# Kernel tuning notes

Hardware: AMD Instinct MI355X
Metric: run time of the kernel (lower is better)

The kernel has to match this reference:

```python
import jax, jax.numpy as jnp
import numpy as np
from jax import lax

RESI_RATIO = 0.5  # abs(quant_resi=-0.5)
BETA = 0.25


def setup_inputs() -> dict:
    key = jax.random.key(0)
    k1, k2, k3, k4 = jax.random.split(key, 4)
    B, C, T, H, W = 2, 32, 8, 32, 32
    V = 8192
    f_BCTHW = jax.random.normal(k1, (B, C, T, H, W), dtype=jnp.float32)
    emb_weight = jax.random.normal(k2, (V, C), dtype=jnp.float32)
    conv_w = jax.random.normal(k3, (C, C, 3, 3, 3), dtype=jnp.float32) * 0.02
    conv_b = jax.random.normal(k4, (C,), dtype=jnp.float32) * 0.02
    return {"f_BCTHW": f_BCTHW, "emb_weight": emb_weight, "conv_w": conv_w, "conv_b": conv_b}


def _mse(a, b):
    d = a - b
    return jnp.mean(d * d)


def reference(f_BCTHW, emb_weight, conv_w, conv_b):
    f = f_BCTHW.astype(jnp.float32)
    B, C, T, H, W = f.shape
    V = emb_weight.shape[0]

    # ---- nearest-codebook assignment (vocab_norm=False path) ----
    # query uses detached f (stop_gradient) exactly as torch .detach()
    q = lax.stop_gradient(f).transpose(0, 2, 3, 4, 1).reshape(-1, C)  # [N, C]
    emb_sg = lax.stop_gradient(emb_weight)
    # ||q||^2 + ||e||^2 - 2 q.e  (addmm_ with alpha=-2, beta=1)
    dist = (jnp.sum(q * q, axis=1, keepdims=True)
            + jnp.sum(emb_sg * emb_sg, axis=1)
            - 2.0 * (q @ emb_sg.T))  # [N, V]
    idx_N = jnp.argmin(dist, axis=1)  # [N] int

    # ---- usage stats (bincount) ----
    counts = jnp.zeros((V,), jnp.float32).at[idx_N].add(1.0)
    prob = counts / jnp.sum(counts)
    vocab_usage = jnp.mean((prob > (0.01 / V)).astype(jnp.float32)) * 100.0

    # ---- embedding gather + residual conv blend ----
    fh = emb_weight[idx_N].reshape(B, T, H, W, C).transpose(0, 4, 1, 2, 3)  # [B,C,T,H,W]
    conv = lax.conv_general_dilated(
        fh, conv_w, window_strides=(1, 1, 1), padding='SAME',
        dimension_numbers=('NCDHW', 'OIDHW', 'NCDHW'))
    conv = conv + conv_b[None, :, None, None, None]
    fh = fh * (1.0 - RESI_RATIO) + conv * RESI_RATIO

    # ---- VQ loss + straight-through estimator ----
    vq_loss = BETA * _mse(lax.stop_gradient(fh), f) + _mse(fh, lax.stop_gradient(f))
    fhat = lax.stop_gradient(fh - f) + f

    return fhat, vq_loss, vocab_usage
```

## Files before the change

kernel.cpp:

```cpp
#include <hip/hip_runtime.h>

#define NQ    16384
#define CDIM  32
#define VSZ   8192
#define PLANE 8192
#define BSTR  262144
#define NEL   524288
#define MARGIN 0.010f
#define NSEG  32
#define GUARD 1088

typedef unsigned long long u64;
typedef unsigned int u32;
typedef unsigned short u16;
using f32x4 = __attribute__((ext_vector_type(4))) float;
using s16x8 = __attribute__((ext_vector_type(8))) short;

__device__ __forceinline__ u32 flip_bits(u32 b) {
    return (b & 0x80000000u) ? ~b : (b | 0x80000000u);
}
__device__ __forceinline__ float unflip_val(u32 b) {
    u32 u = (b & 0x80000000u) ? (b ^ 0x80000000u) : ~b;
    return __uint_as_float(u);
}
__device__ __forceinline__ u16 bf16_rne(float x) {
    u32 u = __float_as_uint(x);
    return (u16)((u + 0x7fffu + ((u >> 16) & 1u)) >> 16);
}

__global__ void k_prep(const float* __restrict__ f, const float* __restrict__ emb,
                       const float* __restrict__ cw,
                       u16* __restrict__ EFh, u16* __restrict__ EFl,
                       u16* __restrict__ QFh, u16* __restrict__ QFl,
                       u16* __restrict__ WFh, u16* __restrict__ WFl,
                       float* __restrict__ enorm, int* __restrict__ counts,
                       int* __restrict__ uct) {
    int t = blockIdx.x * 256 + threadIdx.x;
    if (t < 32768) {
        int tile = t >> 6, l = t & 63;
        int row = tile * 16 + (l & 15);
        int k0 = (l >> 4) * 8;
        const float* src = emb + row * CDIM + k0;
        s16x8 vh, vl;
#pragma unroll
        for (int i = 0; i < 8; ++i) {
            float v = src[i];
            u16 hb = bf16_rne(v);
            float hf = __uint_as_float(((u32)hb) << 16);
            vh[i] = (short)hb;
            vl[i] = (short)bf16_rne(v - hf);
        }
        *(s16x8*)(EFh + t * 8) = vh;
        *(s16x8*)(EFl + t * 8) = vl;
    } else if (t < 98304) {
        int t2 = t - 32768;
        int st = t2 >> 6, l = t2 & 63;
        int n = st * 16 + (l & 15);
        int k0 = (l >> 4) * 8;
        int b = n >> 13, p = n & (PLANE - 1);
        const float* fq = f + b * BSTR + p;
        s16x8 vh, vl;
#pragma unroll
        for (int i = 0; i < 8; ++i) {
            float v = -2.0f * fq[(k0 + i) * PLANE];
            u16 hb = bf16_rne(v);
            float hf = __uint_as_float(((u32)hb) << 16);
            vh[i] = (short)hb;
            vl[i] = (short)bf16_rne(v - hf);
        }
        *(s16x8*)(QFh + t2 * 8) = vh;
        *(s16x8*)(QFl + t2 * 8) = vl;
    } else if (t < 106496) {
        int j = t - 98304;
        const float4* row = (const float4*)(emb + j * CDIM);
        float s = 0.f;
#pragma unroll
        for (int r = 0; r < 8; ++r) {
            float4 v = row[r];
            s += v.x * v.x + v.y * v.y + v.z * v.z + v.w * v.w;
        }
        enorm[j] = s;
        counts[j] = 0;
        if (j == 0) { *uct = 0; }
    } else if (t < 109952) {
        int i = t - 106496;
        int nt = i >> 6, l = i & 63;
        int col = nt * 16 + (l & 15);
        int co = col & 31, u = col >> 5;
        int k0 = (l >> 4) * 8;
        s16x8 vh, vl;
#pragma unroll
        for (int j = 0; j < 8; ++j) {
            int ci = k0 + j;
            float v = cw[co * 864 + ci * 27 + u];
            u16 hb = bf16_rne(v);
            float hf = __uint_as_float(((u32)hb) << 16);
            vh[j] = (short)hb;
            vl[j] = (short)bf16_rne(v - hf);
        }
        *(s16x8*)(WFh + i * 8) = vh;
        *(s16x8*)(WFl + i * 8) = vl;
    }
}

__global__ __launch_bounds__(64) void k_mfma3(
    const u16* __restrict__ QFh, const u16* __restrict__ QFl,
    const u16* __restrict__ EFh, const u16* __restrict__ EFl,
    const float* __restrict__ enorm,
    u64* __restrict__ PARTK, float* __restrict__ PARTM2) {
    const int l = threadIdx.x;
    const int lq = (l >> 4) * 4;
    const int wq = blockIdx.x >> 5, seg = blockIdx.x & 31;

    s16x8 qh[4], ql[4];
#pragma unroll
    for (int s = 0; s < 4; ++s) {
        int st = wq * 4 + s;
        qh[s] = *(const s16x8*)(QFh + (st * 64 + l) * 8);
        ql[s] = *(const s16x8*)(QFl + (st * 64 + l) * 8);
    }
    float m1v[4] = {1e30f, 1e30f, 1e30f, 1e30f};
    float m2v[4] = {1e30f, 1e30f, 1e30f, 1e30f};
    int   m1i[4] = {0, 0, 0, 0};

#pragma unroll 2
    for (int t = 0; t < 16; ++t) {
        int tile = seg * 16 + t;
        s16x8 ah = *(const s16x8*)(EFh + (tile * 64 + l) * 8);
        s16x8 al = *(const s16x8*)(EFl + (tile * 64 + l) * 8);
        f32x4 en = *(const f32x4*)(enorm + tile * 16 + lq);
        int bc = tile * 16 + lq;
#pragma unroll
        for (int s = 0; s < 4; ++s) {
            f32x4 acc = __builtin_amdgcn_mfma_f32_16x16x32_bf16(ah, qh[s], en, 0, 0, 0);
            acc = __builtin_amdgcn_mfma_f32_16x16x32_bf16(ah, ql[s], acc, 0, 0, 0);
            acc = __builtin_amdgcn_mfma_f32_16x16x32_bf16(al, qh[s], acc, 0, 0, 0);
#pragma unroll
            for (int r = 0; r < 4; ++r) {
                float v = acc[r];
                bool lt = v < m1v[s];
                float m2c = fminf(m2v[s], v);
                m2v[s] = lt ? m1v[s] : m2c;
                m1i[s] = lt ? (bc + r) : m1i[s];
                m1v[s] = fminf(m1v[s], v);
            }
        }
    }
#pragma unroll
    for (int s = 0; s < 4; ++s) {
        u64 key = ((u64)flip_bits(__float_as_uint(m1v[s])) << 32) | (u32)m1i[s];
        float m2 = m2v[s];
#pragma unroll
        for (int off = 16; off <= 32; off <<= 1) {
            u64 ko = __shfl_xor(key, off, 64);
            float m2o = __shfl_xor(m2, off, 64);
            u64 kmax = ko > key ? ko : key;
            m2 = fminf(fminf(m2, m2o), unflip_val((u32)(kmax >> 32)));
            key = ko < key ? ko : key;
        }
        if (l < 16) {
            int q = wq * 64 + s * 16 + l;
            PARTK[seg * NQ + q] = key;
            PARTM2[seg * NQ + q] = m2;
        }
    }
}

__global__ void k_final(const u64* __restrict__ PARTK, const float* __restrict__ PARTM2,
                        int* __restrict__ out_idx, int* __restrict__ counts,
                        int* __restrict__ uct, int* __restrict__ ulist) {
    int q = blockIdx.x * 256 + threadIdx.x;
    u64 K = PARTK[q]; float M2 = PARTM2[q];
#pragma unroll
    for (int s = 1; s < NSEG; ++s) {
        u64 k = PARTK[s * NQ + q]; float m2 = PARTM2[s * NQ + q];
        u64 kmax = k > K ? k : K;
        M2 = fminf(fminf(M2, m2), unflip_val((u32)(kmax >> 32)));
        K = k < K ? k : K;
    }
    int idx = (int)(K & 0xffffffffull);
    out_idx[q] = idx;
    float m1 = unflip_val((u32)(K >> 32));
    if (M2 - m1 > MARGIN) {
        atomicAdd(&counts[idx], 1);
    } else {
        int p = atomicAdd(uct, 1);
        ulist[p] = q;
    }
}

__global__ __launch_bounds__(256) void k_exact(
    const int* __restrict__ ulist, const int* __restrict__ uct,
    const float* __restrict__ f, const float* __restrict__ emb,
    const float* __restrict__ enorm, int* __restrict__ out_idx,
    int* __restrict__ counts) {
    __shared__ u64 wred[4][2];
    const int tid = threadIdx.x;
    const int uc = *uct;
    for (int base = blockIdx.x * 2; base < uc; base += 256) {
        int nq = uc - base; if (nq > 2) nq = 2;
        int q0 = ulist[base];
        int q1 = (nq > 1) ? ulist[base + 1] : q0;
        float qv0[CDIM], qv1[CDIM];
        {
            const float* f0 = f + (q0 >> 13) * BSTR + (q0 & (PLANE - 1));
            const float* f1 = f + (q1 >> 13) * BSTR + (q1 & (PLANE - 1));
#pragma unroll
            for (int c = 0; c < CDIM; ++c) {
                qv0[c] = -2.0f * f0[c * PLANE];
                qv1[c] = -2.0f * f1[c * PLANE];
            }
        }
        u64 k0 = ~0ull, k1 = ~0ull;
        for (int jj = 0; jj < 32; ++jj) {
            int j = tid + 256 * jj;
            const float4* er = (const float4*)(emb + j * CDIM);
            float d0 = enorm[j], d1 = d0;
#pragma unroll
            for (int c4 = 0; c4 < 8; ++c4) {
                float4 v = er[c4];
                d0 = fmaf(qv0[c4 * 4 + 0], v.x, d0); d0 = fmaf(qv0[c4 * 4 + 1], v.y, d0);
                d0 = fmaf(qv0[c4 * 4 + 2], v.z, d0); d0 = fmaf(qv0[c4 * 4 + 3], v.w, d0);
                d1 = fmaf(qv1[c4 * 4 + 0], v.x, d1); d1 = fmaf(qv1[c4 * 4 + 1], v.y, d1);
                d1 = fmaf(qv1[c4 * 4 + 2], v.z, d1); d1 = fmaf(qv1[c4 * 4 + 3], v.w, d1);
            }
            u64 nk0 = ((u64)flip_bits(__float_as_uint(d0)) << 32) | (u32)j;
            u64 nk1 = ((u64)flip_bits(__float_as_uint(d1)) << 32) | (u32)j;
            if (nk0 < k0) k0 = nk0;
            if (nk1 < k1) k1 = nk1;
        }
#pragma unroll
        for (int off = 1; off <= 32; off <<= 1) {
            u64 o0 = __shfl_xor(k0, off, 64); if (o0 < k0) k0 = o0;
            u64 o1 = __shfl_xor(k1, off, 64); if (o1 < k1) k1 = o1;
        }
        if ((tid & 63) == 0) { wred[tid >> 6][0] = k0; wred[tid >> 6][1] = k1; }
        __syncthreads();
        if (tid == 0) {
            u64 b0 = wred[0][0], b1 = wred[0][1];
#pragma unroll
            for (int w = 1; w < 4; ++w) {
                if (wred[w][0] < b0) b0 = wred[w][0];
                if (wred[w][1] < b1) b1 = wred[w][1];
            }
            int i0 = (int)(b0 & 0xffffffffull);
            out_idx[q0] = i0; atomicAdd(&counts[i0], 1);
            if (nq > 1) {
                int i1 = (int)(b1 & 0xffffffffull);
                out_idx[q1] = i1; atomicAdd(&counts[i1], 1);
            }
        }
        __syncthreads();
    }
}

__global__ void k_fh2(const int* __restrict__ idx, const float* __restrict__ emb,
                      u16* __restrict__ FH2h, u16* __restrict__ FH2l,
                      const int* __restrict__ counts, float* __restrict__ out) {
    __shared__ int us[4];
    int t = blockIdx.x * 256 + threadIdx.x;
    if (t < NQ) {
        int id = idx[t];
        const float4* e = (const float4*)(emb + id * CDIM);
        s16x8 vh[4], vl[4];
#pragma unroll
        for (int r = 0; r < 8; ++r) {
            float4 v = e[r];
            float vv[4] = {v.x, v.y, v.z, v.w};
#pragma unroll
            for (int j = 0; j < 4; ++j) {
                int q = r * 4 + j;
                u16 hb = bf16_rne(vv[j]);
                float hf = __uint_as_float(((u32)hb) << 16);
                vh[q >> 3][q & 7] = (short)hb;
                vl[q >> 3][q & 7] = (short)bf16_rne(vv[j] - hf);
            }
        }
        u16* dh_ = FH2h + t * CDIM;
        u16* dl_ = FH2l + t * CDIM;
#pragma unroll
        for (int r = 0; r < 4; ++r) {
            *(s16x8*)(dh_ + r * 8) = vh[r];
            *(s16x8*)(dl_ + r * 8) = vl[r];
        }
    } else if (t < 20736) {
        int g = t - NQ;
        int r = g / 1088, off = (g % 1088) * 16;
        u32* dst;
        if (r == 0)      dst = (u32*)(FH2h - GUARD * CDIM);
        else if (r == 1) dst = (u32*)(FH2h + NQ * CDIM);
        else if (r == 2) dst = (u32*)(FH2l - GUARD * CDIM);
        else             dst = (u32*)(FH2l + NQ * CDIM);
#pragma unroll
        for (int i = 0; i < 16; ++i) dst[off + i] = 0;
    } else {
        int tid = threadIdx.x;
        int used = 0;
#pragma unroll
        for (int r = 0; r < 32; ++r) used += (counts[tid + 256 * r] > 0) ? 1 : 0;
#pragma unroll
        for (int off = 32; off > 0; off >>= 1) used += __shfl_down(used, off, 64);
        if ((tid & 63) == 0) us[tid >> 6] = used;
        __syncthreads();
        if (tid == 0) {
            int u = us[0] + us[1] + us[2] + us[3];
            out[NEL + 1] = ((float)u / (float)VSZ) * 100.0f;
        }
    }
}

__global__ __launch_bounds__(192) void k_convm2(
    const u16* __restrict__ FH2h, const u16* __restrict__ FH2l,
    const u16* __restrict__ WFh, const u16* __restrict__ WFl,
    const int* __restrict__ idx, const float* __restrict__ emb,
    const float* __restrict__ bias, const float* __restrict__ f,
    float* __restrict__ out) {
    __shared__ float part[3][64][4];
    const int l = threadIdx.x & 63;
    const int wv = threadIdx.x >> 6;
    const int ntile = blockIdx.x >> 1, cot = blockIdx.x & 1;
    const int co = cot * 16 + (l & 15);
    const int k0 = (l >> 4) * 8;

    const int nA = ntile * 16 + (l & 15);
    const int pA = nA & (PLANE - 1);
    const int tA = pA >> 10, hA = (pA >> 5) & 31, wA = pA & 31;
    const u16* pAh = FH2h + nA * CDIM + k0;
    const u16* pAl = FH2l + nA * CDIM + k0;

    const int ddt = wv - 1;
    const bool okt = ((unsigned)(tA + ddt) < 8u);

    f32x4 a0 = {0.f, 0.f, 0.f, 0.f}, a1 = a0, a2 = a0;
    const s16x8 zf = {0, 0, 0, 0, 0, 0, 0, 0};
#pragma unroll
    for (int v = 0; v < 9; ++v) {
        const int dh = v / 3 - 1, dw = v % 3 - 1;
        const int u = wv * 9 + v;
        const int du = ddt * 1024 + dh * 32 + dw;
        bool ok = okt && ((unsigned)(hA + dh) < 32u) && ((unsigned)(wA + dw) < 32u);
        s16x8 ah = *(const s16x8*)(pAh + du * CDIM);
        s16x8 al = *(const s16x8*)(pAl + du * CDIM);
        if (!ok) { ah = zf; al = zf; }
        int nt = 2 * u + cot;
        s16x8 bh = *(const s16x8*)(WFh + (nt * 64 + l) * 8);
        s16x8 bl = *(const s16x8*)(WFl + (nt * 64 + l) * 8);
        a0 = __builtin_amdgcn_mfma_f32_16x16x32_bf16(ah, bh, a0, 0, 0, 0);
        a1 = __builtin_amdgcn_mfma_f32_16x16x32_bf16(ah, bl, a1, 0, 0, 0);
        a2 = __builtin_amdgcn_mfma_f32_16x16x32_bf16(al, bh, a2, 0, 0, 0);
    }
#pragma unroll
    for (int r = 0; r < 4; ++r) part[wv][l][r] = a0[r] + a1[r] + a2[r];
    __syncthreads();
    if (wv != 0) return;

    f32x4 acc;
#pragma unroll
    for (int r = 0; r < 4; ++r)
        acc[r] = part[0][l][r] + part[1][l][r] + part[2][l][r];
    const float bv = bias[co];

    const int n0 = ntile * 16 + (l >> 4) * 4;
    const int b = n0 >> 13, p0 = n0 & (PLANE - 1);
    const long fb = (long)b * BSTR + (long)co * PLANE + p0;
    const float4 f4 = *(const float4*)(f + fb);
    const int4 iv = *(const int4*)(idx + n0);
    float o0 = 0.5f * emb[iv.x * CDIM + co] + 0.5f * (acc[0] + bv);
    float o1 = 0.5f * emb[iv.y * CDIM + co] + 0.5f * (acc[1] + bv);
    float o2 = 0.5f * emb[iv.z * CDIM + co] + 0.5f * (acc[2] + bv);
    float o3 = 0.5f * emb[iv.w * CDIM + co] + 0.5f * (acc[3] + bv);
    float4 o4 = {o0, o1, o2, o3};
    *(float4*)(out + fb) = o4;
    float d0 = o0 - f4.x, d1 = o1 - f4.y, d2 = o2 - f4.z, d3 = o3 - f4.w;
    float s = fmaf(d0, d0, fmaf(d1, d1, fmaf(d2, d2, d3 * d3)));
#pragma unroll
    for (int off = 32; off > 0; off >>= 1) s += __shfl_down(s, off, 64);
    if (l == 0) atomicAdd(out + NEL, s * (1.25f / (float)NEL));
}

extern "C" void kernel_launch(void* const* d_in, const int* in_sizes, int n_in,
                              void* d_out, int out_size, void* d_ws, size_t ws_size,
                              hipStream_t stream) {
    const float* f      = (const float*)d_in[0];
    const float* emb    = (const float*)d_in[1];
    const float* conv_w = (const float*)d_in[2];
    const float* conv_b = (const float*)d_in[3];
    float* out = (float*)d_out;
    float* ws = (float*)d_ws;

    float* enorm    = ws;
    int*   counts   = (int*)(ws + 8192);
    int*   idxb     = (int*)(ws + 16384);
    int*   uct      = (int*)(ws + 32769);
    int*   ulist    = (int*)(ws + 32772);
    u16*   EFh      = (u16*)(ws + 49408);
    u16*   EFl      = (u16*)(ws + 180480);
    u16*   QFh      = (u16*)(ws + 311552);
    u16*   QFl      = (u16*)(ws + 573696);
    u16*   WFh      = (u16*)(ws + 835840);
    u16*   WFl      = (u16*)(ws + 842752);
    u64*   PARTK    = (u64*)(ws + 849664);
    float* PARTM2   = ws + 1898240;
    u16*   FH2h     = (u16*)(ws + 849664)  + GUARD * CDIM;
    u16*   FH2l     = (u16*)(ws + 1146624) + GUARD * CDIM;

    k_prep   <<<430, 256, 0, stream>>>(f, emb, conv_w, EFh, EFl, QFh, QFl,
                                       WFh, WFl, enorm, counts, uct);
    k_mfma3  <<<8192, 64, 0, stream>>>(QFh, QFl, EFh, EFl, enorm, PARTK, PARTM2);
    k_final  <<<64, 256, 0, stream>>>(PARTK, PARTM2, idxb, counts, uct, ulist);
    k_exact  <<<128, 256, 0, stream>>>(ulist, uct, f, emb, enorm, idxb, counts);
    k_fh2    <<<82, 256, 0, stream>>>(idxb, emb, FH2h, FH2l, counts, out);
    k_convm2 <<<2048, 192, 0, stream>>>(FH2h, FH2l, WFh, WFl, idxb, emb,
                                        conv_b, f, out);
}
```

Before: 183.2 us.

## Fuse exact-recheck pass into final reduction kernel with per-block shared uncertain list

```diff
diff --git a/kernel.cpp b/kernel.cpp
--- a/kernel.cpp
+++ b/kernel.cpp
@@ -33,8 +33,7 @@
                        u16* __restrict__ EFh, u16* __restrict__ EFl,
                        u16* __restrict__ QFh, u16* __restrict__ QFl,
                        u16* __restrict__ WFh, u16* __restrict__ WFl,
-                       float* __restrict__ enorm, int* __restrict__ counts,
-                       int* __restrict__ uct) {
+                       float* __restrict__ enorm, int* __restrict__ counts) {
     int t = blockIdx.x * 256 + threadIdx.x;
     if (t < 32768) {
         int tile = t >> 6, l = t & 63;
@@ -81,7 +80,6 @@
         }
         enorm[j] = s;
         counts[j] = 0;
-        if (j == 0) { *uct = 0; }
     } else if (t < 109952) {
         int i = t - 106496;
         int nt = i >> 6, l = i & 63;
@@ -166,10 +164,19 @@
     }
 }
 
-__global__ void k_final(const u64* __restrict__ PARTK, const float* __restrict__ PARTM2,
-                        int* __restrict__ out_idx, int* __restrict__ counts,
-                        int* __restrict__ uct, int* __restrict__ ulist) {
-    int q = blockIdx.x * 256 + threadIdx.x;
+__global__ __launch_bounds__(256) void k_finalx(
+    const u64* __restrict__ PARTK, const float* __restrict__ PARTM2,
+    const float* __restrict__ f, const float* __restrict__ emb,
+    const float* __restrict__ enorm,
+    int* __restrict__ out_idx, int* __restrict__ counts) {
+    __shared__ int ulist_s[256];
+    __shared__ int ucnt_s;
+    __shared__ u64 wred[4];
+    const int tid = threadIdx.x;
+    if (tid == 0) ucnt_s = 0;
+    __syncthreads();
+
+    int q = blockIdx.x * 256 + tid;
     u64 K = PARTK[q]; float M2 = PARTM2[q];
 #pragma unroll
     for (int s = 1; s < NSEG; ++s) {
@@ -184,71 +191,45 @@
     if (M2 - m1 > MARGIN) {
         atomicAdd(&counts[idx], 1);
     } else {
-        int p = atomicAdd(uct, 1);
-        ulist[p] = q;
-    }
-}
-
-__global__ __launch_bounds__(256) void k_exact(
-    const int* __restrict__ ulist, const int* __restrict__ uct,
-    const float* __restrict__ f, const float* __restrict__ emb,
-    const float* __restrict__ enorm, int* __restrict__ out_idx,
-    int* __restrict__ counts) {
-    __shared__ u64 wred[4][2];
-    const int tid = threadIdx.x;
-    const int uc = *uct;
-    for (int base = blockIdx.x * 2; base < uc; base += 256) {
-        int nq = uc - base; if (nq > 2) nq = 2;
-        int q0 = ulist[base];
-        int q1 = (nq > 1) ? ulist[base + 1] : q0;
-        float qv0[CDIM], qv1[CDIM];
-        {
-            const float* f0 = f + (q0 >> 13) * BSTR + (q0 & (PLANE - 1));
-            const float* f1 = f + (q1 >> 13) * BSTR + (q1 & (PLANE - 1));
-#pragma unroll
-            for (int c = 0; c < CDIM; ++c) {
-                qv0[c] = -2.0f * f0[c * PLANE];
-                qv1[c] = -2.0f * f1[c * PLANE];
-            }
-        }
-        u64 k0 = ~0ull, k1 = ~0ull;
+        int p = atomicAdd(&ucnt_s, 1);
+        ulist_s[p] = q;
+    }
+    __syncthreads();
+
+    const int uc = ucnt_s;
+    for (int i = 0; i < uc; ++i) {
+        int qu = ulist_s[i];
+        const float* fq = f + (qu >> 13) * BSTR + (qu & (PLANE - 1));
+        float qv[CDIM];
+#pragma unroll
+        for (int c = 0; c < CDIM; ++c) qv[c] = -2.0f * fq[c * PLANE];
+        u64 k0 = ~0ull;
         for (int jj = 0; jj < 32; ++jj) {
             int j = tid + 256 * jj;
             const float4* er = (const float4*)(emb + j * CDIM);
-            float d0 = enorm[j], d1 = d0;
+            float d0 = enorm[j];
 #pragma unroll
             for (int c4 = 0; c4 < 8; ++c4) {
                 float4 v = er[c4];
-                d0 = fmaf(qv0[c4 * 4 + 0], v.x, d0); d0 = fmaf(qv0[c4 * 4 + 1], v.y, d0);
-                d0 = fmaf(qv0[c4 * 4 + 2], v.z, d0); d0 = fmaf(qv0[c4 * 4 + 3], v.w, d0);
-                d1 = fmaf(qv1[c4 * 4 + 0], v.x, d1); d1 = fmaf(qv1[c4 * 4 + 1], v.y, d1);
-                d1 = fmaf(qv1[c4 * 4 + 2], v.z, d1); d1 = fmaf(qv1[c4 * 4 + 3], v.w, d1);
+                d0 = fmaf(qv[c4 * 4 + 0], v.x, d0); d0 = fmaf(qv[c4 * 4 + 1], v.y, d0);
+                d0 = fmaf(qv[c4 * 4 + 2], v.z, d0); d0 = fmaf(qv[c4 * 4 + 3], v.w, d0);
             }
-            u64 nk0 = ((u64)flip_bits(__float_as_uint(d0)) << 32) | (u32)j;
-            u64 nk1 = ((u64)flip_bits(__float_as_uint(d1)) << 32) | (u32)j;
-            if (nk0 < k0) k0 = nk0;
-            if (nk1 < k1) k1 = nk1;
+            u64 nk = ((u64)flip_bits(__float_as_uint(d0)) << 32) | (u32)j;
+            if (nk < k0) k0 = nk;
         }
 #pragma unroll
         for (int off = 1; off <= 32; off <<= 1) {
             u64 o0 = __shfl_xor(k0, off, 64); if (o0 < k0) k0 = o0;
-            u64 o1 = __shfl_xor(k1, off, 64); if (o1 < k1) k1 = o1;
-        }
-        if ((tid & 63) == 0) { wred[tid >> 6][0] = k0; wred[tid >> 6][1] = k1; }
+        }
+        if ((tid & 63) == 0) wred[tid >> 6] = k0;
         __syncthreads();
         if (tid == 0) {
-            u64 b0 = wred[0][0], b1 = wred[0][1];
-#pragma unroll
-            for (int w = 1; w < 4; ++w) {
-                if (wred[w][0] < b0) b0 = wred[w][0];
-                if (wred[w][1] < b1) b1 = wred[w][1];
-            }
+            u64 b0 = wred[0];
+#pragma unroll
+            for (int w = 1; w < 4; ++w) if (wred[w] < b0) b0 = wred[w];
             int i0 = (int)(b0 & 0xffffffffull);
-            out_idx[q0] = i0; atomicAdd(&counts[i0], 1);
-            if (nq > 1) {
-                int i1 = (int)(b1 & 0xffffffffull);
-                out_idx[q1] = i1; atomicAdd(&counts[i1], 1);
-            }
+            out_idx[qu] = i0;
+            atomicAdd(&counts[i0], 1);
         }
         __syncthreads();
     }
@@ -391,8 +372,6 @@
     float* enorm    = ws;
     int*   counts   = (int*)(ws + 8192);
     int*   idxb     = (int*)(ws + 16384);
-    int*   uct      = (int*)(ws + 32769);
-    int*   ulist    = (int*)(ws + 32772);
     u16*   EFh      = (u16*)(ws + 49408);
     u16*   EFl      = (u16*)(ws + 180480);
     u16*   QFh      = (u16*)(ws + 311552);
@@ -405,10 +384,9 @@
     u16*   FH2l     = (u16*)(ws + 1146624) + GUARD * CDIM;
 
     k_prep   <<<430, 256, 0, stream>>>(f, emb, conv_w, EFh, EFl, QFh, QFl,
-                                       WFh, WFl, enorm, counts, uct);
+                                       WFh, WFl, enorm, counts);
     k_mfma3  <<<8192, 64, 0, stream>>>(QFh, QFl, EFh, EFl, enorm, PARTK, PARTM2);
-    k_final  <<<64, 256, 0, stream>>>(PARTK, PARTM2, idxb, counts, uct, ulist);
-    k_exact  <<<128, 256, 0, stream>>>(ulist, uct, f, emb, enorm, idxb, counts);
+    k_finalx <<<64, 256, 0, stream>>>(PARTK, PARTM2, f, emb, enorm, idxb, counts);
     k_fh2    <<<82, 256, 0, stream>>>(idxb, emb, FH2h, FH2l, counts, out);
     k_convm2 <<<2048, 192, 0, stream>>>(FH2h, FH2l, WFh, WFl, idxb, emb,
                                         conv_b, f, out);
```

New measurement: 320.8 us. 1.75x slower.
